# Kernel optimization log

Measured on AMD Instinct MI355X. Metric: run time of the kernel, lower is better.

Reference implementation:

```python
import jax, jax.numpy as jnp
import numpy as np

N, E, F_IN, H, L, G, NH, HD, C = 50000, 640000, 64, 128, 3, 64, 8, 16, 2


def setup_inputs() -> dict:
    key = jax.random.key(0)
    k = jax.random.split(key, 12)
    s = 0.02
    return {
        "x": jax.random.normal(k[0], (N, F_IN), jnp.float32),
        "edge_index": jax.random.randint(k[1], (2, E), 0, N),
        "batch_idx": jnp.sort(jax.random.randint(k[2], (N,), 0, G)),
        "emb_w": jax.random.normal(k[3], (H, F_IN), jnp.float32) * s,
        "emb_b": jnp.zeros((H,), jnp.float32),
        "gcn_w": jax.random.normal(k[4], (L, H, H), jnp.float32) * s,
        "gcn_b": jnp.zeros((L, H), jnp.float32),
        "lstm_w_ih": jax.random.normal(k[5], (4 * H, H), jnp.float32) * s,
        "lstm_w_hh": jax.random.normal(k[6], (4 * H, H), jnp.float32) * s,
        "lstm_b_ih": jnp.zeros((4 * H,), jnp.float32),
        "lstm_b_hh": jnp.zeros((4 * H,), jnp.float32),
        "attn_in_w": jax.random.normal(k[7], (3 * H, H), jnp.float32) * s,
        "attn_in_b": jnp.zeros((3 * H,), jnp.float32),
        "attn_out_w": jax.random.normal(k[8], (H, H), jnp.float32) * s,
        "attn_out_b": jnp.zeros((H,), jnp.float32),
        "cls_w1": jax.random.normal(k[9], (H // 2, H), jnp.float32) * s,
        "cls_b1": jnp.zeros((H // 2,), jnp.float32),
        "cls_w2": jax.random.normal(k[10], (C, H // 2), jnp.float32) * s,
        "cls_b2": jnp.zeros((C,), jnp.float32),
    }


def reference(x, edge_index, batch_idx, emb_w, emb_b, gcn_w, gcn_b,
              lstm_w_ih, lstm_w_hh, lstm_b_ih, lstm_b_hh,
              attn_in_w, attn_in_b, attn_out_w, attn_out_b,
              cls_w1, cls_b1, cls_w2, cls_b2):
    src, dst = edge_index[0], edge_index[1]
    # GCN symmetric norm with self-loops (PyG gcn_norm): deg includes the self loop
    deg = jax.ops.segment_sum(jnp.ones((E,), x.dtype), dst, num_segments=N) + 1.0
    dis = jax.lax.rsqrt(deg)                      # deg^{-1/2}, deg >= 1
    norm = dis[src] * dis[dst]                    # [E]
    self_norm = dis * dis                         # [N], self-loop weight

    h = x @ emb_w.T + emb_b                       # node embedding [N, H]
    for l in range(L):
        hw = h @ gcn_w[l].T                       # linear transform [N, H]
        agg = jax.ops.segment_sum(hw[src] * norm[:, None], dst, num_segments=N)
        agg = agg + hw * self_norm[:, None]       # self-loop contribution
        h = jax.nn.relu(agg + gcn_b[l])

    # global mean pool per graph
    sums = jax.ops.segment_sum(h, batch_idx, num_segments=G)
    counts = jax.ops.segment_sum(jnp.ones((N,), h.dtype), batch_idx, num_segments=G)
    ge = sums / jnp.maximum(counts, 1.0)[:, None]  # [G, H]

    # LSTM with seq_len=1, h0=c0=0 (W_hh term vanishes); gate order i,f,g,o
    gates = ge @ lstm_w_ih.T + lstm_b_ih + lstm_b_hh
    i, f, g, o = jnp.split(gates, 4, axis=-1)
    c = jax.nn.sigmoid(i) * jnp.tanh(g)
    hs = jax.nn.sigmoid(o) * jnp.tanh(c)           # [G, H]

    # MultiheadAttention, seq_len=1 self-attention
    q, kk, v = jnp.split(hs @ attn_in_w.T + attn_in_b, 3, axis=-1)
    qh = q.reshape(G, NH, HD)
    kh = kk.reshape(G, NH, HD)
    vh = v.reshape(G, NH, HD)
    scores = jnp.einsum('bhd,bhd->bh', qh, kh) / jnp.sqrt(jnp.asarray(HD, hs.dtype))
    attn = jax.nn.softmax(scores[..., None], axis=-1)[..., 0]  # single key -> all ones
    ctx = (attn[..., None] * vh).reshape(G, H)
    fe = ctx @ attn_out_w.T + attn_out_b           # attended_out.mean(dim=1) with S=1

    # classifier (dropout is identity at inference)
    z = jax.nn.relu(fe @ cls_w1.T + cls_b1)
    return z @ cls_w2.T + cls_b2
```

## Files before the change

kernel.cpp:

```cpp
#include <hip/hip_runtime.h>
#include <math.h>

#define N_NODES 50000
#define N_EDGES 640000
#define F_INDIM 64
#define HDIM 128
#define NLAYERS 3
#define NGRAPH 64
#define NCLS 2
#define SCAN_BLOCKS ((N_NODES + 255) / 256)
#define POOL_SPLIT 8
#define NTILES (N_NODES / 16)

typedef __attribute__((ext_vector_type(8))) short bf16x8;
typedef __attribute__((ext_vector_type(4))) float f32x4;

__device__ __forceinline__ float bf_lo(unsigned v) { return __uint_as_float(v << 16); }
__device__ __forceinline__ float bf_hi(unsigned v) { return __uint_as_float(v & 0xffff0000u); }
__device__ __forceinline__ unsigned short f2bf(float f) {
    unsigned b = __float_as_uint(f);
    return (unsigned short)((b + 0x7fffu + ((b >> 16) & 1u)) >> 16);
}


__global__ __launch_bounds__(256) void k_init(int* hist, float* pool, float* counts) {
    int i = blockIdx.x * 256 + threadIdx.x;
    if (i < N_NODES) hist[i] = 0;
    if (i < NGRAPH * HDIM) pool[i] = 0.f;
    if (i < NGRAPH) counts[i] = 0.f;
}

__global__ __launch_bounds__(256) void k_hist(const int* __restrict__ dst, int* __restrict__ hist) {
    int e = blockIdx.x * 256 + threadIdx.x;
    if (e < N_EDGES) atomicAdd(&hist[dst[e]], 1);
}

__global__ __launch_bounds__(256) void k_scan1(const int* __restrict__ hist,
                                               int* __restrict__ row_start,
                                               int* __restrict__ partials,
                                               float* __restrict__ dis) {
    __shared__ int buf[256];
    int i = blockIdx.x * 256 + threadIdx.x;
    int v = (i < N_NODES) ? hist[i] : 0;
    if (i < N_NODES) dis[i] = rsqrtf((float)v + 1.0f);
    buf[threadIdx.x] = v;
    __syncthreads();
#pragma unroll
    for (int off = 1; off < 256; off <<= 1) {
        int t = (threadIdx.x >= off) ? buf[threadIdx.x - off] : 0;
        __syncthreads();
        buf[threadIdx.x] += t;
        __syncthreads();
    }
    if (i < N_NODES) row_start[i] = buf[threadIdx.x] - v;
    if (threadIdx.x == 255) partials[blockIdx.x] = buf[255];
}

__global__ __launch_bounds__(256) void k_scan2(int* __restrict__ partials) {
    __shared__ int buf[256];
    int v = (threadIdx.x < SCAN_BLOCKS) ? partials[threadIdx.x] : 0;
    buf[threadIdx.x] = v;
    __syncthreads();
#pragma unroll
    for (int off = 1; off < 256; off <<= 1) {
        int t = (threadIdx.x >= off) ? buf[threadIdx.x - off] : 0;
        __syncthreads();
        buf[threadIdx.x] += t;
        __syncthreads();
    }
    if (threadIdx.x < SCAN_BLOCKS) partials[threadIdx.x] = buf[threadIdx.x] - v;
}

__global__ __launch_bounds__(256) void k_scan3(int* __restrict__ row_start,
                                               const int* __restrict__ partials,
                                               int* __restrict__ cursor) {
    int i = blockIdx.x * 256 + threadIdx.x;
    if (i < N_NODES) {
        int r = row_start[i] + partials[blockIdx.x];
        row_start[i] = r;
        cursor[i] = r;
    }
    if (i == 0) row_start[N_NODES] = N_EDGES;
}

__global__ __launch_bounds__(256) void k_scatter(const int* __restrict__ src,
                                                 const int* __restrict__ dst,
                                                 const float* __restrict__ dis,
                                                 int* __restrict__ cursor,
                                                 uint2* __restrict__ csr) {
    int e = blockIdx.x * 256 + threadIdx.x;
    if (e >= N_EDGES) return;
    int s = src[e], d = dst[e];
    int pos = atomicAdd(&cursor[d], 1);
    uint2 rec;
    rec.x = (unsigned)s;
    rec.y = __float_as_uint(dis[s] * dis[d]);
    csr[pos] = rec;
}


__global__ __launch_bounds__(256) void k_cvt(const float* __restrict__ src,
                                             unsigned short* __restrict__ dst, int n4) {
    int i = blockIdx.x * 256 + threadIdx.x;
    if (i >= n4) return;
    float4 v = *(const float4*)&src[i * 4];
    unsigned r0 = (unsigned)f2bf(v.x) | ((unsigned)f2bf(v.y) << 16);
    unsigned r1 = (unsigned)f2bf(v.z) | ((unsigned)f2bf(v.w) << 16);
    *(uint2*)&dst[i * 4] = make_uint2(r0, r1);
}


template<int K>
__global__ __launch_bounds__(256) void k_mm(const unsigned short* __restrict__ A,
                                            const unsigned short* __restrict__ W,
                                            const float* __restrict__ bias,
                                            unsigned short* __restrict__ C) {
    constexpr int KS = K / 32;
    int lane = threadIdx.x & 63;
    int lg = lane >> 4, lr = lane & 15;
    int cb = (threadIdx.x >> 6) * 32;
    int tile0 = blockIdx.x * 4;

    bf16x8 wf[2][KS];
#pragma unroll
    for (int ct = 0; ct < 2; ++ct)
#pragma unroll
        for (int ks = 0; ks < KS; ++ks)
            wf[ct][ks] = *(const bf16x8*)&W[(size_t)(cb + ct * 16 + lr) * K + ks * 32 + lg * 8];

    float b0 = bias ? bias[cb + lr] : 0.f;
    float b1 = bias ? bias[cb + 16 + lr] : 0.f;

    int ntile = NTILES - tile0; if (ntile > 4) ntile = 4;
    for (int t = 0; t < ntile; ++t) {
        int rb = (tile0 + t) * 16;
        f32x4 acc0 = {0.f, 0.f, 0.f, 0.f}, acc1 = {0.f, 0.f, 0.f, 0.f};
#pragma unroll
        for (int ks = 0; ks < KS; ++ks) {
            bf16x8 af = *(const bf16x8*)&A[(size_t)(rb + lr) * K + ks * 32 + lg * 8];
            acc0 = __builtin_amdgcn_mfma_f32_16x16x32_bf16(af, wf[0][ks], acc0, 0, 0, 0);
            acc1 = __builtin_amdgcn_mfma_f32_16x16x32_bf16(af, wf[1][ks], acc1, 0, 0, 0);
        }
        int row = rb + lg * 4;
#pragma unroll
        for (int j = 0; j < 4; ++j) {
            C[(size_t)(row + j) * HDIM + cb + lr]      = f2bf(acc0[j] + b0);
            C[(size_t)(row + j) * HDIM + cb + 16 + lr] = f2bf(acc1[j] + b1);
        }
    }
}


__global__ __launch_bounds__(256) void k_gather(const unsigned short* __restrict__ hw,
                                                const int* __restrict__ row_start,
                                                const uint2* __restrict__ csr,
                                                const float* __restrict__ dis,
                                                const float* __restrict__ bias,
                                                unsigned short* __restrict__ hout) {
    int n = blockIdx.x * 4 + (threadIdx.x >> 6);
    int lane = threadIdx.x & 63;
    int half = lane >> 5;
    int cl = lane & 31;
    int beg = row_start[n], end = row_start[n + 1];
    float a0 = 0.f, a1 = 0.f, a2 = 0.f, a3 = 0.f;
    int e = beg;
    for (; e + 8 <= end; e += 8) {
        uint2 rec[4]; uint2 v[4];
#pragma unroll
        for (int u = 0; u < 4; ++u)
            rec[u] = csr[e + 2 * u + half];
#pragma unroll
        for (int u = 0; u < 4; ++u)
            v[u] = *(const uint2*)&hw[(size_t)rec[u].x * HDIM + cl * 4];
#pragma unroll
        for (int u = 0; u < 4; ++u) {
            float w = __uint_as_float(rec[u].y);
            a0 += w * bf_lo(v[u].x);
            a1 += w * bf_hi(v[u].x);
            a2 += w * bf_lo(v[u].y);
            a3 += w * bf_hi(v[u].y);
        }
    }
    for (; e < end; e += 2) {
        int me = e + half;
        bool valid = me < end;
        uint2 rec = valid ? csr[me] : make_uint2((unsigned)n, 0u);
        uint2 v = *(const uint2*)&hw[(size_t)rec.x * HDIM + cl * 4];
        float w = __uint_as_float(rec.y);
        a0 += w * bf_lo(v.x); a1 += w * bf_hi(v.x);
        a2 += w * bf_lo(v.y); a3 += w * bf_hi(v.y);
    }
    a0 += __shfl_xor(a0, 32); a1 += __shfl_xor(a1, 32);
    a2 += __shfl_xor(a2, 32); a3 += __shfl_xor(a3, 32);
    if (half == 0) {
        float dn = dis[n], sn = dn * dn;
        uint2 vs = *(const uint2*)&hw[(size_t)n * HDIM + cl * 4];
        a0 += sn * bf_lo(vs.x); a1 += sn * bf_hi(vs.x);
        a2 += sn * bf_lo(vs.y); a3 += sn * bf_hi(vs.y);
        float4 b = *(const float4*)&bias[cl * 4];
        a0 = fmaxf(a0 + b.x, 0.f); a1 = fmaxf(a1 + b.y, 0.f);
        a2 = fmaxf(a2 + b.z, 0.f); a3 = fmaxf(a3 + b.w, 0.f);
        uint2 r;
        r.x = (unsigned)f2bf(a0) | ((unsigned)f2bf(a1) << 16);
        r.y = (unsigned)f2bf(a2) | ((unsigned)f2bf(a3) << 16);
        *(uint2*)&hout[(size_t)n * HDIM + cl * 4] = r;
    }
}


__global__ __launch_bounds__(256) void k_pool(const unsigned short* __restrict__ h,
                                              const int* __restrict__ batch,
                                              float* __restrict__ pool,
                                              float* __restrict__ counts) {
    int g  = blockIdx.x >> 3;
    int sp = blockIdx.x & 7;
    int s, e;
    {
        int lo = 0, hi = N_NODES;
        while (lo < hi) { int mid = (lo + hi) >> 1; if (batch[mid] < g) lo = mid + 1; else hi = mid; }
        s = lo;
        lo = s; hi = N_NODES;
        while (lo < hi) { int mid = (lo + hi) >> 1; if (batch[mid] < g + 1) lo = mid + 1; else hi = mid; }
        e = lo;
    }
    int len = e - s;
    int chunk = (len + POOL_SPLIT - 1) / POOL_SPLIT;
    int ss = s + sp * chunk;
    int ee = min(ss + chunk, e);
    int cp = threadIdx.x & 63;
    int r  = threadIdx.x >> 6;
    float a0 = 0.f, a1 = 0.f;
    for (int n = ss + r; n < ee; n += 4) {
        unsigned v = *(const unsigned*)&h[(size_t)n * HDIM + cp * 2];
        a0 += bf_lo(v);
        a1 += bf_hi(v);
    }
    __shared__ float red0[4][64], red1[4][64];
    red0[r][cp] = a0; red1[r][cp] = a1;
    __syncthreads();
    if (r == 0) {
#pragma unroll
        for (int j = 1; j < 4; ++j) { a0 += red0[j][cp]; a1 += red1[j][cp]; }
        atomicAdd(&pool[g * HDIM + cp * 2], a0);
        atomicAdd(&pool[g * HDIM + cp * 2 + 1], a1);
    }
    if (threadIdx.x == 0 && ee > ss) atomicAdd(&counts[g], (float)(ee - ss));
}


__global__ __launch_bounds__(128) void k_tail(const float* __restrict__ pool,
                                              const float* __restrict__ counts,
                                              const float* __restrict__ w_ih,
                                              const float* __restrict__ b_ih,
                                              const float* __restrict__ b_hh,
                                              const float* __restrict__ attn_in_w,
                                              const float* __restrict__ attn_in_b,
                                              const float* __restrict__ attn_out_w,
                                              const float* __restrict__ attn_out_b,
                                              const float* __restrict__ w1,
                                              const float* __restrict__ b1,
                                              const float* __restrict__ w2,
                                              const float* __restrict__ b2,
                                              float* __restrict__ out) {
    __shared__ float ge[128], hsr[128], vv[128], fe[128], zz[64];
    int g = blockIdx.x, t = threadIdx.x;
    float cnt = fmaxf(counts[g], 1.0f);
    ge[t] = pool[g * HDIM + t] / cnt;
    __syncthreads();
    float gi = 0.f, gg = 0.f, go = 0.f;
    for (int k = 0; k < 128; ++k) {
        float xv = ge[k];
        gi += xv * w_ih[t * HDIM + k];
        gg += xv * w_ih[(256 + t) * HDIM + k];
        go += xv * w_ih[(384 + t) * HDIM + k];
    }
    gi += b_ih[t] + b_hh[t];
    gg += b_ih[256 + t] + b_hh[256 + t];
    go += b_ih[384 + t] + b_hh[384 + t];
    float cc = (1.f / (1.f + expf(-gi))) * tanhf(gg);
    float hv = (1.f / (1.f + expf(-go))) * tanhf(cc);
    hsr[t] = hv;
    __syncthreads();
    float va = attn_in_b[256 + t];
    for (int k = 0; k < 128; ++k) va += hsr[k] * attn_in_w[(256 + t) * HDIM + k];
    vv[t] = va;
    __syncthreads();
    float fv = attn_out_b[t];
    for (int k = 0; k < 128; ++k) fv += vv[k] * attn_out_w[t * HDIM + k];
    fe[t] = fv;
    __syncthreads();
    if (t < 64) {
        float zv = b1[t];
        for (int k = 0; k < 128; ++k) zv += fe[k] * w1[t * HDIM + k];
        zz[t] = fmaxf(zv, 0.f);
    }
    __syncthreads();
    if (t < NCLS) {
        float ov = b2[t];
        for (int k = 0; k < 64; ++k) ov += zz[k] * w2[t * 64 + k];
        out[g * NCLS + t] = ov;
    }
}


extern "C" void kernel_launch(void* const* d_in, const int* in_sizes, int n_in,
                              void* d_out, int out_size, void* d_ws, size_t ws_size,
                              hipStream_t stream) {
    const float* x          = (const float*)d_in[0];
    const int*   edge_index = (const int*)d_in[1];
    const int*   batch      = (const int*)d_in[2];
    const float* emb_w      = (const float*)d_in[3];
    const float* emb_b      = (const float*)d_in[4];
    const float* gcn_w      = (const float*)d_in[5];
    const float* gcn_b      = (const float*)d_in[6];
    const float* w_ih       = (const float*)d_in[7];
    const float* b_ih       = (const float*)d_in[9];
    const float* b_hh       = (const float*)d_in[10];
    const float* attn_in_w  = (const float*)d_in[11];
    const float* attn_in_b  = (const float*)d_in[12];
    const float* attn_out_w = (const float*)d_in[13];
    const float* attn_out_b = (const float*)d_in[14];
    const float* w1         = (const float*)d_in[15];
    const float* b1         = (const float*)d_in[16];
    const float* w2         = (const float*)d_in[17];
    const float* b2         = (const float*)d_in[18];
    float* out = (float*)d_out;

    int*   iws = (int*)d_ws;
    float* fws = (float*)d_ws;
    int*   hist      = iws;
    float* dis       = fws + N_NODES;
    int*   row_start = iws + 2 * N_NODES;
    int*   cursor    = iws + 3 * N_NODES + 4;
    uint2* csr       = (uint2*)(iws + 4 * N_NODES + 8);
    unsigned short* bws   = (unsigned short*)(iws + 4 * N_NODES + 8 + 2 * N_EDGES);
    unsigned short* x_bf  = bws;
    unsigned short* we_bf = x_bf + (size_t)N_NODES * F_INDIM;
    unsigned short* wg_bf = we_bf + HDIM * F_INDIM;
    unsigned short* hA    = wg_bf + NLAYERS * HDIM * HDIM;
    unsigned short* hB    = hA + (size_t)N_NODES * HDIM;
    float* pool     = (float*)(hB + (size_t)N_NODES * HDIM);
    float* counts   = pool + NGRAPH * HDIM;
    int*   partials = (int*)(counts + NGRAPH);

    const int* src = edge_index;
    const int* dst = edge_index + N_EDGES;

    k_init<<<196, 256, 0, stream>>>(hist, pool, counts);
    k_hist<<<(N_EDGES + 255) / 256, 256, 0, stream>>>(dst, hist);
    k_scan1<<<SCAN_BLOCKS, 256, 0, stream>>>(hist, row_start, partials, dis);
    k_scan2<<<1, 256, 0, stream>>>(partials);
    k_scan3<<<SCAN_BLOCKS, 256, 0, stream>>>(row_start, partials, cursor);
    k_scatter<<<(N_EDGES + 255) / 256, 256, 0, stream>>>(src, dst, dis, cursor, csr);

    k_cvt<<<(N_NODES * F_INDIM / 4 + 255) / 256, 256, 0, stream>>>(x, x_bf, N_NODES * F_INDIM / 4);
    k_cvt<<<(HDIM * F_INDIM / 4 + 255) / 256, 256, 0, stream>>>(emb_w, we_bf, HDIM * F_INDIM / 4);
    k_cvt<<<(NLAYERS * HDIM * HDIM / 4 + 255) / 256, 256, 0, stream>>>(gcn_w, wg_bf, NLAYERS * HDIM * HDIM / 4);

    int mm_grid = (NTILES + 3) / 4;
    k_mm<F_INDIM><<<mm_grid, 256, 0, stream>>>(x_bf, we_bf, emb_b, hA);
    for (int l = 0; l < NLAYERS; ++l) {
        k_mm<HDIM><<<mm_grid, 256, 0, stream>>>(hA, wg_bf + l * HDIM * HDIM, nullptr, hB);
        k_gather<<<N_NODES / 4, 256, 0, stream>>>(hB, row_start, csr, dis,
                                                  gcn_b + l * HDIM, hA);
    }
    k_pool<<<NGRAPH * POOL_SPLIT, 256, 0, stream>>>(hA, batch, pool, counts);
    k_tail<<<NGRAPH, 128, 0, stream>>>(pool, counts, w_ih, b_ih, b_hh,
                                       attn_in_w, attn_in_b, attn_out_w, attn_out_b,
                                       w1, b1, w2, b2, out);
}
```

Before: 284.7 us.

## Build CSR with per-edge ranks instead of second atomic pass; unroll gather deeper

The histogram pass now records each edge's rank within its destination via the atomicAdd return value, so the placement pass writes to row_start[d]+rank[e] with no atomics and the cursor array and its init are dropped. The gather kernel gains a 16-edge unrolled loop with 8 outstanding loads per half-wave to raise memory-level parallelism. The cost is an extra 640K-int rank array written and read, plus more registers in the gather kernel.

```diff
diff --git a/kernel.cpp b/kernel.cpp
--- a/kernel.cpp
+++ b/kernel.cpp
@@ -23,16 +23,18 @@
 }
 
 
-__global__ __launch_bounds__(256) void k_init(int* hist, float* pool, float* counts) {
+__global__ __launch_bounds__(256) void k_init(int* cnt, float* pool, float* counts) {
     int i = blockIdx.x * 256 + threadIdx.x;
-    if (i < N_NODES) hist[i] = 0;
+    if (i < N_NODES) cnt[i] = 0;
     if (i < NGRAPH * HDIM) pool[i] = 0.f;
     if (i < NGRAPH) counts[i] = 0.f;
 }
 
-__global__ __launch_bounds__(256) void k_hist(const int* __restrict__ dst, int* __restrict__ hist) {
+__global__ __launch_bounds__(256) void k_rank(const int* __restrict__ dst,
+                                              int* __restrict__ cnt,
+                                              int* __restrict__ rank) {
     int e = blockIdx.x * 256 + threadIdx.x;
-    if (e < N_EDGES) atomicAdd(&hist[dst[e]], 1);
+    if (e < N_EDGES) rank[e] = atomicAdd(&cnt[dst[e]], 1);
 }
 
 __global__ __launch_bounds__(256) void k_scan1(const int* __restrict__ hist,
@@ -72,30 +74,25 @@
 }
 
 __global__ __launch_bounds__(256) void k_scan3(int* __restrict__ row_start,
-                                               const int* __restrict__ partials,
-                                               int* __restrict__ cursor) {
+                                               const int* __restrict__ partials) {
     int i = blockIdx.x * 256 + threadIdx.x;
-    if (i < N_NODES) {
-        int r = row_start[i] + partials[blockIdx.x];
-        row_start[i] = r;
-        cursor[i] = r;
-    }
+    if (i < N_NODES) row_start[i] += partials[blockIdx.x];
     if (i == 0) row_start[N_NODES] = N_EDGES;
 }
 
-__global__ __launch_bounds__(256) void k_scatter(const int* __restrict__ src,
-                                                 const int* __restrict__ dst,
-                                                 const float* __restrict__ dis,
-                                                 int* __restrict__ cursor,
-                                                 uint2* __restrict__ csr) {
+__global__ __launch_bounds__(256) void k_place(const int* __restrict__ src,
+                                               const int* __restrict__ dst,
+                                               const int* __restrict__ rank,
+                                               const float* __restrict__ dis,
+                                               const int* __restrict__ row_start,
+                                               uint2* __restrict__ csr) {
     int e = blockIdx.x * 256 + threadIdx.x;
     if (e >= N_EDGES) return;
     int s = src[e], d = dst[e];
-    int pos = atomicAdd(&cursor[d], 1);
     uint2 rec;
     rec.x = (unsigned)s;
     rec.y = __float_as_uint(dis[s] * dis[d]);
-    csr[pos] = rec;
+    csr[row_start[d] + rank[e]] = rec;
 }
 
 
@@ -164,6 +161,23 @@
     int beg = row_start[n], end = row_start[n + 1];
     float a0 = 0.f, a1 = 0.f, a2 = 0.f, a3 = 0.f;
     int e = beg;
+    for (; e + 16 <= end; e += 16) {
+        uint2 rec[8]; uint2 v[8];
+#pragma unroll
+        for (int u = 0; u < 8; ++u)
+            rec[u] = csr[e + 2 * u + half];
+#pragma unroll
+        for (int u = 0; u < 8; ++u)
+            v[u] = *(const uint2*)&hw[(size_t)rec[u].x * HDIM + cl * 4];
+#pragma unroll
+        for (int u = 0; u < 8; ++u) {
+            float w = __uint_as_float(rec[u].y);
+            a0 += w * bf_lo(v[u].x);
+            a1 += w * bf_hi(v[u].x);
+            a2 += w * bf_lo(v[u].y);
+            a3 += w * bf_hi(v[u].y);
+        }
+    }
     for (; e + 8 <= end; e += 8) {
         uint2 rec[4]; uint2 v[4];
 #pragma unroll
@@ -328,12 +342,12 @@
 
     int*   iws = (int*)d_ws;
     float* fws = (float*)d_ws;
-    int*   hist      = iws;
+    int*   cnt       = iws;
     float* dis       = fws + N_NODES;
     int*   row_start = iws + 2 * N_NODES;
-    int*   cursor    = iws + 3 * N_NODES + 4;
-    uint2* csr       = (uint2*)(iws + 4 * N_NODES + 8);
-    unsigned short* bws   = (unsigned short*)(iws + 4 * N_NODES + 8 + 2 * N_EDGES);
+    int*   rank      = iws + 3 * N_NODES + 4;
+    uint2* csr       = (uint2*)(iws + 3 * N_NODES + 4 + N_EDGES);
+    unsigned short* bws   = (unsigned short*)(iws + 3 * N_NODES + 4 + N_EDGES + 2 * N_EDGES);
     unsigned short* x_bf  = bws;
     unsigned short* we_bf = x_bf + (size_t)N_NODES * F_INDIM;
     unsigned short* wg_bf = we_bf + HDIM * F_INDIM;
@@ -346,12 +360,12 @@
     const int* src = edge_index;
     const int* dst = edge_index + N_EDGES;
 
-    k_init<<<196, 256, 0, stream>>>(hist, pool, counts);
-    k_hist<<<(N_EDGES + 255) / 256, 256, 0, stream>>>(dst, hist);
-    k_scan1<<<SCAN_BLOCKS, 256, 0, stream>>>(hist, row_start, partials, dis);
+    k_init<<<196, 256, 0, stream>>>(cnt, pool, counts);
+    k_rank<<<(N_EDGES + 255) / 256, 256, 0, stream>>>(dst, cnt, rank);
+    k_scan1<<<SCAN_BLOCKS, 256, 0, stream>>>(cnt, row_start, partials, dis);
     k_scan2<<<1, 256, 0, stream>>>(partials);
-    k_scan3<<<SCAN_BLOCKS, 256, 0, stream>>>(row_start, partials, cursor);
-    k_scatter<<<(N_EDGES + 255) / 256, 256, 0, stream>>>(src, dst, dis, cursor, csr);
+    k_scan3<<<SCAN_BLOCKS, 256, 0, stream>>>(row_start, partials);
+    k_place<<<(N_EDGES + 255) / 256, 256, 0, stream>>>(src, dst, rank, dis, row_start, csr);
 
     k_cvt<<<(N_NODES * F_INDIM / 4 + 255) / 256, 256, 0, stream>>>(x, x_bf, N_NODES * F_INDIM / 4);
     k_cvt<<<(HDIM * F_INDIM / 4 + 255) / 256, 256, 0, stream>>>(emb_w, we_bf, HDIM * F_INDIM / 4);
```

After: 267.2 us. 6.1% less time.
